# Optimization experiments

Hardware: AMD Instinct MI355X
Metric: run time of the kernel (lower is better)

Reference implementation:

```python
import jax, jax.numpy as jnp
import numpy as np

N = 32767      # 2**15 - 1 nodes: complete binary tree, parent(i) = (i-1)//2
IN = 512       # in_channels
H = 256        # hidden_dim
OUT = 1        # output_dim
DEPTH = 15     # number of topological levels (static)


def setup_inputs() -> dict:
    key = jax.random.key(0)
    ks = jax.random.split(key, 8)
    x = jax.random.normal(ks[0], (N, IN), dtype=jnp.float32)
    # complete binary tree edge list: edge_index[0]=child, edge_index[1]=parent
    src = jnp.arange(1, N, dtype=jnp.int32)
    dst = (src - 1) // 2
    edge_index = jnp.stack([src, dst])  # [2, N-1]
    s = 1.0 / np.sqrt(H)  # torch LSTMCell/Linear default uniform init scale
    W_ih = jax.random.uniform(ks[1], (4 * H, IN), minval=-s, maxval=s, dtype=jnp.float32)
    W_hh = jax.random.uniform(ks[2], (4 * H, H), minval=-s, maxval=s, dtype=jnp.float32)
    b_ih = jax.random.uniform(ks[3], (4 * H,), minval=-s, maxval=s, dtype=jnp.float32)
    b_hh = jax.random.uniform(ks[4], (4 * H,), minval=-s, maxval=s, dtype=jnp.float32)
    W_fc = jax.random.uniform(ks[5], (OUT, H), minval=-s, maxval=s, dtype=jnp.float32)
    b_fc = jax.random.uniform(ks[6], (OUT,), minval=-s, maxval=s, dtype=jnp.float32)
    return {"x": x, "edge_index": edge_index, "W_ih": W_ih, "W_hh": W_hh,
            "b_ih": b_ih, "b_hh": b_hh, "W_fc": W_fc, "b_fc": b_fc}


def reference(x, edge_index, W_ih, W_hh, b_ih, b_hh, W_fc, b_fc):
    src, dst = edge_index[0], edge_index[1]
    # children count per parent (matches torch children_count loop)
    cnt = jax.ops.segment_sum(jnp.ones_like(src, dtype=x.dtype), dst, num_segments=N)
    cnt = jnp.maximum(cnt, 1.0)[:, None]  # [N,1]; leaves get zero child state anyway
    h = jnp.zeros((N, H), dtype=x.dtype)
    c = jnp.zeros((N, H), dtype=x.dtype)
    # topological sweep: deepest level first (children processed before parents)
    for d in range(DEPTH - 1, -1, -1):
        lo = 2 ** d - 1
        hi = min(2 ** (d + 1) - 1, N)  # level d node index range (static)
        # mean of already-computed child h/c states, gathered via edge list
        mean_h = jax.ops.segment_sum(h[src], dst, num_segments=N)[lo:hi] / cnt[lo:hi]
        mean_c = jax.ops.segment_sum(c[src], dst, num_segments=N)[lo:hi] / cnt[lo:hi]
        # torch LSTMCell: gates in (i, f, g, o) order
        gates = x[lo:hi] @ W_ih.T + b_ih + mean_h @ W_hh.T + b_hh  # [n_level, 4H]
        i, f, g, o = jnp.split(gates, 4, axis=-1)
        i, f, o = jax.nn.sigmoid(i), jax.nn.sigmoid(f), jax.nn.sigmoid(o)
        g = jnp.tanh(g)
        c_new = f * mean_c + i * g
        h_new = o * jnp.tanh(c_new)
        h = h.at[lo:hi].set(h_new)
        c = c.at[lo:hi].set(c_new)
    pooled = jnp.mean(h, axis=0, keepdims=True)  # [1, H]
    out = pooled @ W_fc.T + b_fc                 # [1, 1]
    return out.squeeze(-1)                       # [1]
```

## Files before the change

### kernel.cpp

```cpp
#include <hip/hip_runtime.h>
#include <math.h>


#define N_NODES 32767
#define N_LEAF0 16383
#define IN_C    512
#define H_C     256

typedef __bf16 bf16x8 __attribute__((ext_vector_type(8)));
typedef __bf16 bf16x4 __attribute__((ext_vector_type(4)));
typedef float  f32x4  __attribute__((ext_vector_type(4)));

__device__ __forceinline__ void gload_lds16(const void* g, void* l) {
    __builtin_amdgcn_global_load_lds(
        (const __attribute__((address_space(1))) unsigned int*)g,
        (__attribute__((address_space(3))) unsigned int*)l,
        16, 0, 0);
}

__device__ __forceinline__ float fast_rcp(float x) { return __builtin_amdgcn_rcpf(x); }
__device__ __forceinline__ float sigm(float x)     { return fast_rcp(1.f + __expf(-x)); }
__device__ __forceinline__ float tanh_fast(float x){ return 2.f * fast_rcp(1.f + __expf(-2.f * x)) - 1.f; }

__global__ __launch_bounds__(256)
void conv_weights(const float* __restrict__ wih, const float* __restrict__ whh,
                  __bf16* __restrict__ wihb, __bf16* __restrict__ whh2)
{
    const int i = blockIdx.x * 256 + threadIdx.x;
    const float* src; __bf16* dst; float scale; int j;
    if (i < 65536) { src = wih; dst = wihb; scale = 1.0f; j = i; }
    else           { src = whh; dst = whh2; scale = 0.5f; j = i - 65536; }
    const float4* s4 = (const float4*)src;
    const float4 a = s4[2 * j];
    const float4 b = s4[2 * j + 1];
    bf16x8 o;
    o[0] = (__bf16)(scale * a.x); o[1] = (__bf16)(scale * a.y);
    o[2] = (__bf16)(scale * a.z); o[3] = (__bf16)(scale * a.w);
    o[4] = (__bf16)(scale * b.x); o[5] = (__bf16)(scale * b.y);
    o[6] = (__bf16)(scale * b.z); o[7] = (__bf16)(scale * b.w);
    *(bf16x8*)(dst + 8 * j) = o;
}

__global__ __launch_bounds__(256, 2)
void bulk_xw(const float* __restrict__ x,
             const __bf16* __restrict__ wihb,
             const float* __restrict__ b_ih,
             const float* __restrict__ b_hh,
             __bf16* __restrict__ hb,
             __bf16* __restrict__ cb_,
             __bf16* __restrict__ gx)
{
    __shared__ __bf16 As[16 * 64 * 32];

    const int t    = threadIdx.x;
    const int lane = t & 63;
    const int wv   = t >> 6;
    const int quad = lane >> 4;
    const int l15  = lane & 15;
    const int m0   = blockIdx.x * 64;

    {
        const int r  = t >> 2;
        const int ks = (t & 3) * 128;
        const int node = min(m0 + r, N_NODES - 1);
        const float* xr = x + (size_t)node * IN_C + ks;
#pragma unroll
        for (int j = 0; j < 16; ++j) {
            const int k = ks + j * 8;
            const float4 a = *(const float4*)(xr + j * 8);
            const float4 b = *(const float4*)(xr + j * 8 + 4);
            bf16x8 o;
            o[0] = (__bf16)a.x; o[1] = (__bf16)a.y; o[2] = (__bf16)a.z; o[3] = (__bf16)a.w;
            o[4] = (__bf16)b.x; o[5] = (__bf16)b.y; o[6] = (__bf16)b.z; o[7] = (__bf16)b.w;
            *(bf16x8*)(As + (k >> 5) * 2048 + r * 32 + (k & 31)) = o;
        }
    }
    __syncthreads();

    for (int sp = 0; sp < 4; ++sp) {
        const int s  = sp * 4 + wv;
        const int CH = s * 16 + l15;
        float bs[4];
#pragma unroll
        for (int q = 0; q < 4; ++q) bs[q] = b_ih[q * H_C + CH] + b_hh[q * H_C + CH];

        f32x4 acc[4][4];
#pragma unroll
        for (int mi = 0; mi < 4; ++mi)
#pragma unroll
            for (int ni = 0; ni < 4; ++ni) acc[mi][ni] = (f32x4)0.f;

#pragma unroll 4
        for (int kc = 0; kc < 16; ++kc) {
            bf16x8 af[4], bfr[4];
#pragma unroll
            for (int mi = 0; mi < 4; ++mi)
                af[mi] = *(const bf16x8*)(As + kc * 2048 + (mi * 16 + l15) * 32 + quad * 8);
#pragma unroll
            for (int ni = 0; ni < 4; ++ni) {
                const int grow = ni * 256 + s * 16 + l15;
                bfr[ni] = *(const bf16x8*)(wihb + (size_t)grow * IN_C + kc * 32 + quad * 8);
            }
#pragma unroll
            for (int mi = 0; mi < 4; ++mi)
#pragma unroll
                for (int ni = 0; ni < 4; ++ni)
                    acc[mi][ni] = __builtin_amdgcn_mfma_f32_16x16x32_bf16(
                        af[mi], bfr[ni], acc[mi][ni], 0, 0, 0);
        }

#pragma unroll
        for (int mi = 0; mi < 4; ++mi) {
#pragma unroll
            for (int r = 0; r < 4; ++r) {
                const int m = m0 + mi * 16 + quad * 4 + r;
                if (m >= N_NODES) continue;
                if (m >= N_LEAF0) {
                    const float gi = sigm(acc[mi][0][r] + bs[0]);
                    const float gg = tanh_fast(acc[mi][2][r] + bs[2]);
                    const float go = sigm(acc[mi][3][r] + bs[3]);
                    const float cn = gi * gg;
                    const float hn = go * tanh_fast(cn);
                    cb_[(size_t)m * H_C + CH] = (__bf16)cn;
                    hb[(size_t)m * H_C + CH] = (__bf16)hn;
                } else {
                    bf16x4 g4;
#pragma unroll
                    for (int q = 0; q < 4; ++q) g4[q] = (__bf16)acc[mi][q][r];
                    *(bf16x4*)(gx + (size_t)m * 1024 + CH * 4) = g4;
                }
            }
        }
    }
}

__global__ __launch_bounds__(256)
void level_hw(const __bf16* __restrict__ whh2,
              const float* __restrict__ b_ih,
              const float* __restrict__ b_hh,
              const __bf16* __restrict__ gx,
              __bf16* __restrict__ hb,
              __bf16* __restrict__ cb_,
              int lo, int n)
{
    __shared__ __bf16 Bfull[8 * 128 * 32];

    const int t    = threadIdx.x;
    const int lane = t & 63;
    const int wv   = t >> 6;
    const int wm   = wv >> 1;
    const int wn   = wv & 1;
    const int quad = lane >> 4;
    const int l15  = lane & 15;
    const int bx   = blockIdx.x;
    const int cb   = bx & 7;
    const int m0   = (bx >> 3) * 128;

#pragma unroll
    for (int kc = 0; kc < 8; ++kc) {
#pragma unroll
        for (int e = 0; e < 2; ++e) {
            const int chunk = wv * 2 + e;
            const int nl    = chunk * 16 + (lane >> 2);
            const int q     = (nl >> 4) & 3;
            const int cc    = (nl & 15) + ((nl >> 6) << 4);
            const int grow  = q * H_C + cb * 32 + cc;
            const void* g = (const char*)(whh2 + grow * H_C + kc * 32) + (lane & 3) * 16;
            gload_lds16(g, (char*)Bfull + kc * 8192 + chunk * 1024);
        }
    }
    __syncthreads();

    f32x4 acc[4][4];
#pragma unroll
    for (int mi = 0; mi < 4; ++mi)
#pragma unroll
        for (int ni = 0; ni < 4; ++ni) acc[mi][ni] = (f32x4)0.f;

    size_t abase[4];
#pragma unroll
    for (int mi = 0; mi < 4; ++mi) {
        const int node = lo + m0 + wm * 64 + mi * 16 + l15;
        abase[mi] = (size_t)(2 * node + 1) * H_C;
    }

#pragma unroll
    for (int kc = 0; kc < 16; ++kc) {
        bf16x8 af[4], bfr[4];
#pragma unroll
        for (int mi = 0; mi < 4; ++mi)
            af[mi] = *(const bf16x8*)(hb + abase[mi] + kc * 32 + quad * 8);
#pragma unroll
        for (int ni = 0; ni < 4; ++ni)
            bfr[ni] = *(const bf16x8*)(Bfull + (kc & 7) * 4096 +
                                       (wn * 64 + ni * 16 + l15) * 32 + quad * 8);
#pragma unroll
        for (int mi = 0; mi < 4; ++mi)
#pragma unroll
            for (int ni = 0; ni < 4; ++ni)
                acc[mi][ni] = __builtin_amdgcn_mfma_f32_16x16x32_bf16(
                    af[mi], bfr[ni], acc[mi][ni], 0, 0, 0);
    }

    const int CH = cb * 32 + wn * 16 + l15;
    const float bs0 = b_ih[0 * H_C + CH] + b_hh[0 * H_C + CH];
    const float bs1 = b_ih[1 * H_C + CH] + b_hh[1 * H_C + CH];
    const float bs2 = b_ih[2 * H_C + CH] + b_hh[2 * H_C + CH];
    const float bs3 = b_ih[3 * H_C + CH] + b_hh[3 * H_C + CH];

#pragma unroll
    for (int mi = 0; mi < 4; ++mi) {
#pragma unroll
        for (int r = 0; r < 4; ++r) {
            const int m = m0 + wm * 64 + mi * 16 + quad * 4 + r;
            if (m < n) {
                const int node = lo + m;
                const bf16x4 g4 = *(const bf16x4*)(gx + (size_t)node * 1024 + CH * 4);
                const float gi = sigm(acc[mi][0][r] + (float)g4[0] + bs0);
                const float gf = sigm(acc[mi][1][r] + (float)g4[1] + bs1);
                const float gt = tanh_fast(acc[mi][2][r] + (float)g4[2] + bs2);
                const float go = sigm(acc[mi][3][r] + (float)g4[3] + bs3);
                const float mc = 0.5f * ((float)cb_[(size_t)(2 * node + 1) * H_C + CH] +
                                         (float)cb_[(size_t)(2 * node + 2) * H_C + CH]);
                const float cn = gf * mc + gi * gt;
                const float hn = go * tanh_fast(cn);
                cb_[(size_t)node * H_C + CH] = (__bf16)cn;
                hb[(size_t)node * H_C + CH] = (__bf16)hn;
            }
        }
    }
}

__global__ __launch_bounds__(256)
void levels_tail(const __bf16* __restrict__ whh2,
                 const float* __restrict__ b_ih,
                 const float* __restrict__ b_hh,
                 const __bf16* __restrict__ gx,
                 __bf16* __restrict__ hb,
                 __bf16* __restrict__ cb_,
                 int* __restrict__ bar)
{
    const int t    = threadIdx.x;
    const int lane = t & 63;
    const int wv   = t >> 6;
    const int wm   = wv >> 1;
    const int wn   = wv & 1;
    const int quad = lane >> 4;
    const int l15  = lane & 15;
    const int b    = blockIdx.x;
    const int slab = b & 7;
    const int mg   = b >> 3;

    const int CH = slab * 32 + wn * 16 + l15;
    const float bs0 = b_ih[0 * H_C + CH] + b_hh[0 * H_C + CH];
    const float bs1 = b_ih[1 * H_C + CH] + b_hh[1 * H_C + CH];
    const float bs2 = b_ih[2 * H_C + CH] + b_hh[2 * H_C + CH];
    const float bs3 = b_ih[3 * H_C + CH] + b_hh[3 * H_C + CH];

    int target = 0;

    for (int d = 9; d >= 0; --d) {
        const int n  = 1 << d;
        const int lo = n - 1;
        if (mg * 64 < n) {
            const int m0 = mg * 64;

            f32x4 acc[2][4];
#pragma unroll
            for (int mi = 0; mi < 2; ++mi)
#pragma unroll
                for (int ni = 0; ni < 4; ++ni) acc[mi][ni] = (f32x4)0.f;

            size_t abase[2];
#pragma unroll
            for (int mi = 0; mi < 2; ++mi) {
                const int node = lo + m0 + wm * 32 + mi * 16 + l15;
                abase[mi] = (size_t)(2 * node + 1) * H_C;
            }

#pragma unroll 4
            for (int kc = 0; kc < 16; ++kc) {
                bf16x8 af[2], bfr[4];
#pragma unroll
                for (int mi = 0; mi < 2; ++mi)
                    af[mi] = *(const bf16x8*)(hb + abase[mi] + kc * 32 + quad * 8);
#pragma unroll
                for (int ni = 0; ni < 4; ++ni) {
                    const int grow = ni * H_C + CH;
                    bfr[ni] = *(const bf16x8*)(whh2 + (size_t)grow * H_C +
                                               (kc & 7) * 32 + quad * 8);
                }
#pragma unroll
                for (int mi = 0; mi < 2; ++mi)
#pragma unroll
                    for (int ni = 0; ni < 4; ++ni)
                        acc[mi][ni] = __builtin_amdgcn_mfma_f32_16x16x32_bf16(
                            af[mi], bfr[ni], acc[mi][ni], 0, 0, 0);
            }

#pragma unroll
            for (int mi = 0; mi < 2; ++mi) {
#pragma unroll
                for (int r = 0; r < 4; ++r) {
                    const int m = m0 + wm * 32 + mi * 16 + quad * 4 + r;
                    if (m < n) {
                        const int node = lo + m;
                        const bf16x4 g4 = *(const bf16x4*)(gx + (size_t)node * 1024 + CH * 4);
                        const float gi = sigm(acc[mi][0][r] + (float)g4[0] + bs0);
                        const float gf = sigm(acc[mi][1][r] + (float)g4[1] + bs1);
                        const float gt = tanh_fast(acc[mi][2][r] + (float)g4[2] + bs2);
                        const float go = sigm(acc[mi][3][r] + (float)g4[3] + bs3);
                        const float mc = 0.5f * ((float)cb_[(size_t)(2 * node + 1) * H_C + CH] +
                                                 (float)cb_[(size_t)(2 * node + 2) * H_C + CH]);
                        const float cn = gf * mc + gi * gt;
                        const float hn = go * tanh_fast(cn);
                        cb_[(size_t)node * H_C + CH] = (__bf16)cn;
                        hb[(size_t)node * H_C + CH] = (__bf16)hn;
                    }
                }
            }
        }

        if (d > 0) {
            __syncthreads();
            target += 64;
            if (t == 0) {
                __threadfence();
                atomicAdd(bar, 1);
                while (__hip_atomic_load(bar, __ATOMIC_RELAXED,
                                         __HIP_MEMORY_SCOPE_AGENT) < target)
                    __builtin_amdgcn_s_sleep(8);
                __threadfence();
            }
            __syncthreads();
        }
    }
}

__global__ __launch_bounds__(256)
void reduce_rows(const __bf16* __restrict__ hb, float* __restrict__ part)
{
    const int tcol = threadIdx.x;
    const int b = blockIdx.x;
    float s = 0.f;
    for (int r = 0; r < 128; ++r) {
        const int row = b * 128 + r;
        if (row < N_NODES) s += (float)hb[(size_t)row * H_C + tcol];
    }
    part[b * H_C + tcol] = s;
}

__global__ __launch_bounds__(256)
void reduce_final(const float* __restrict__ part,
                  const float* __restrict__ W_fc,
                  const float* __restrict__ b_fc,
                  float* __restrict__ out)
{
    __shared__ float sm[256];
    const int t = threadIdx.x;
    float s = 0.f;
    for (int j = 0; j < 256; ++j) s += part[j * H_C + t];
    s = s * (1.0f / (float)N_NODES) * W_fc[t];
    sm[t] = s;
    __syncthreads();
    for (int st = 128; st > 0; st >>= 1) {
        if (t < st) sm[t] += sm[t + st];
        __syncthreads();
    }
    if (t == 0) out[0] = sm[0] + b_fc[0];
}

extern "C" void kernel_launch(void* const* d_in, const int* in_sizes, int n_in,
                              void* d_out, int out_size, void* d_ws, size_t ws_size,
                              hipStream_t stream)
{
    const float* x    = (const float*)d_in[0];
    const float* W_ih = (const float*)d_in[2];
    const float* W_hh = (const float*)d_in[3];
    const float* b_ih = (const float*)d_in[4];
    const float* b_hh = (const float*)d_in[5];
    const float* W_fc = (const float*)d_in[6];
    const float* b_fc = (const float*)d_in[7];
    float* out = (float*)d_out;

    char* w = (char*)d_ws;
    __bf16* hb   = (__bf16*)w;  w += (size_t)N_NODES * H_C * 2;
    __bf16* cb_  = (__bf16*)w;  w += (size_t)N_NODES * H_C * 2;
    __bf16* gx   = (__bf16*)w;  w += (size_t)N_LEAF0 * 1024 * 2;
    __bf16* wihb = (__bf16*)w;  w += (size_t)4 * H_C * IN_C * 2;
    __bf16* whh2 = (__bf16*)w;  w += (size_t)4 * H_C * H_C * 2;
    float*  part = (float*)w;   w += (size_t)256 * H_C * 4;
    int*    bar  = (int*)w;

    hipMemsetAsync(bar, 0, sizeof(int), stream);

    conv_weights<<<384, 256, 0, stream>>>(W_ih, W_hh, wihb, whh2);

    bulk_xw<<<512, 256, 0, stream>>>(x, wihb, b_ih, b_hh, hb, cb_, gx);

    for (int d = 13; d >= 10; --d) {
        const int n  = 1 << d;
        const int lo = n - 1;
        const int nm = n / 128;
        level_hw<<<8 * nm, 256, 0, stream>>>(whh2, b_ih, b_hh, gx, hb, cb_, lo, n);
    }

    levels_tail<<<64, 256, 0, stream>>>(whh2, b_ih, b_hh, gx, hb, cb_, bar);

    reduce_rows<<<256, 256, 0, stream>>>(hb, part);
    reduce_final<<<1, 256, 0, stream>>>(part, W_fc, b_fc, out);
}
```

Before: 455.8 us.

## Fold level 10 into persistent tail kernel and use relaxed atomics instead of fences

Level 10 now runs inside the persistent levels_tail kernel, which launches 128 blocks instead of 64, so one fewer separate level_hw launch is needed. The grid barrier drops its __threadfence calls and sleeps for a shorter interval. Cross-block visibility of h/c now relies on agent-scope relaxed atomic loads and stores of the bf16 state. This cuts launch and fence overhead, but relaxed atomics without fences give weak ordering guarantees, and the split 8-byte and 2-byte atomic accesses may be less efficient than plain vector loads.

```diff
diff --git a/kernel.cpp b/kernel.cpp
--- a/kernel.cpp
+++ b/kernel.cpp
@@ -10,6 +10,9 @@
 typedef __bf16 bf16x8 __attribute__((ext_vector_type(8)));
 typedef __bf16 bf16x4 __attribute__((ext_vector_type(4)));
 typedef float  f32x4  __attribute__((ext_vector_type(4)));
+
+union U64B { unsigned long long u; bf16x4 v; };
+union U16B { unsigned short u; __bf16 b; };
 
 __device__ __forceinline__ void gload_lds16(const void* g, void* l) {
     __builtin_amdgcn_global_load_lds(
@@ -21,6 +24,28 @@
 __device__ __forceinline__ float fast_rcp(float x) { return __builtin_amdgcn_rcpf(x); }
 __device__ __forceinline__ float sigm(float x)     { return fast_rcp(1.f + __expf(-x)); }
 __device__ __forceinline__ float tanh_fast(float x){ return 2.f * fast_rcp(1.f + __expf(-2.f * x)) - 1.f; }
+
+__device__ __forceinline__ bf16x8 aload16(const __bf16* p) {
+    U64B a, b;
+    a.u = __hip_atomic_load((const unsigned long long*)p,
+                            __ATOMIC_RELAXED, __HIP_MEMORY_SCOPE_AGENT);
+    b.u = __hip_atomic_load((const unsigned long long*)(p + 4),
+                            __ATOMIC_RELAXED, __HIP_MEMORY_SCOPE_AGENT);
+    bf16x8 r;
+    r[0]=a.v[0]; r[1]=a.v[1]; r[2]=a.v[2]; r[3]=a.v[3];
+    r[4]=b.v[0]; r[5]=b.v[1]; r[6]=b.v[2]; r[7]=b.v[3];
+    return r;
+}
+__device__ __forceinline__ float aload_bf16(const __bf16* p) {
+    U16B u; u.u = __hip_atomic_load((const unsigned short*)p,
+                                    __ATOMIC_RELAXED, __HIP_MEMORY_SCOPE_AGENT);
+    return (float)u.b;
+}
+__device__ __forceinline__ void astore_bf16(__bf16* p, float v) {
+    U16B u; u.b = (__bf16)v;
+    __hip_atomic_store((unsigned short*)p, u.u,
+                       __ATOMIC_RELAXED, __HIP_MEMORY_SCOPE_AGENT);
+}
 
 __global__ __launch_bounds__(256)
 void conv_weights(const float* __restrict__ wih, const float* __restrict__ whh,
@@ -259,7 +284,7 @@
 
     int target = 0;
 
-    for (int d = 9; d >= 0; --d) {
+    for (int d = 10; d >= 0; --d) {
         const int n  = 1 << d;
         const int lo = n - 1;
         if (mg * 64 < n) {
@@ -283,7 +308,7 @@
                 bf16x8 af[2], bfr[4];
 #pragma unroll
                 for (int mi = 0; mi < 2; ++mi)
-                    af[mi] = *(const bf16x8*)(hb + abase[mi] + kc * 32 + quad * 8);
+                    af[mi] = aload16(hb + abase[mi] + kc * 32 + quad * 8);
 #pragma unroll
                 for (int ni = 0; ni < 4; ++ni) {
                     const int grow = ni * H_C + CH;
@@ -310,12 +335,13 @@
                         const float gf = sigm(acc[mi][1][r] + (float)g4[1] + bs1);
                         const float gt = tanh_fast(acc[mi][2][r] + (float)g4[2] + bs2);
                         const float go = sigm(acc[mi][3][r] + (float)g4[3] + bs3);
-                        const float mc = 0.5f * ((float)cb_[(size_t)(2 * node + 1) * H_C + CH] +
-                                                 (float)cb_[(size_t)(2 * node + 2) * H_C + CH]);
+                        const float mc = 0.5f *
+                            (aload_bf16(cb_ + (size_t)(2 * node + 1) * H_C + CH) +
+                             aload_bf16(cb_ + (size_t)(2 * node + 2) * H_C + CH));
                         const float cn = gf * mc + gi * gt;
                         const float hn = go * tanh_fast(cn);
-                        cb_[(size_t)node * H_C + CH] = (__bf16)cn;
-                        hb[(size_t)node * H_C + CH] = (__bf16)hn;
+                        astore_bf16(cb_ + (size_t)node * H_C + CH, cn);
+                        astore_bf16(hb + (size_t)node * H_C + CH, hn);
                     }
                 }
             }
@@ -323,14 +349,12 @@
 
         if (d > 0) {
             __syncthreads();
-            target += 64;
+            target += 128;
             if (t == 0) {
-                __threadfence();
                 atomicAdd(bar, 1);
                 while (__hip_atomic_load(bar, __ATOMIC_RELAXED,
                                          __HIP_MEMORY_SCOPE_AGENT) < target)
-                    __builtin_amdgcn_s_sleep(8);
-                __threadfence();
+                    __builtin_amdgcn_s_sleep(2);
             }
             __syncthreads();
         }
@@ -398,14 +422,14 @@
 
     bulk_xw<<<512, 256, 0, stream>>>(x, wihb, b_ih, b_hh, hb, cb_, gx);
 
-    for (int d = 13; d >= 10; --d) {
+    for (int d = 13; d >= 11; --d) {
         const int n  = 1 << d;
         const int lo = n - 1;
         const int nm = n / 128;
         level_hw<<<8 * nm, 256, 0, stream>>>(whh2, b_ih, b_hh, gx, hb, cb_, lo, n);
     }
 
-    levels_tail<<<64, 256, 0, stream>>>(whh2, b_ih, b_hh, gx, hb, cb_, bar);
+    levels_tail<<<128, 256, 0, stream>>>(whh2, b_ih, b_hh, gx, hb, cb_, bar);
 
     reduce_rows<<<256, 256, 0, stream>>>(hb, part);
     reduce_final<<<1, 256, 0, stream>>>(part, W_fc, b_fc, out);
```

Result: slower. 484.3 us (+6.2%).

## Process tree levels as independent subtrees per block instead of per-level launches

Applied to the files above, without the earlier changes.

Replaces the four per-level launches and the grid-barrier tail kernel with a subtree decomposition. Each of 128 blocks handles its own subtree rooted at level 7 through levels 13 to 7, staging child h rows in LDS. A single 1024-thread block then finishes levels 6 to 0. This removes launch overhead and the atomic grid barrier, but the mid kernel now uses only 128 blocks and loops over all 8 column slabs serially, reading W_hh from global memory. That risks underusing the GPU on the wide levels (8192 nodes at level 13) that previously ran with many blocks.

```diff
diff --git a/kernel.cpp b/kernel.cpp
--- a/kernel.cpp
+++ b/kernel.cpp
@@ -6,6 +6,7 @@
 #define N_LEAF0 16383
 #define IN_C    512
 #define H_C     256
+#define AST     520
 
 typedef __bf16 bf16x8 __attribute__((ext_vector_type(8)));
 typedef __bf16 bf16x4 __attribute__((ext_vector_type(4)));
@@ -134,87 +135,56 @@
     }
 }
 
-__global__ __launch_bounds__(256)
-void level_hw(const __bf16* __restrict__ whh2,
-              const float* __restrict__ b_ih,
-              const float* __restrict__ b_hh,
-              const __bf16* __restrict__ gx,
-              __bf16* __restrict__ hb,
-              __bf16* __restrict__ cb_,
-              int lo, int n)
-{
-    __shared__ __bf16 Bfull[8 * 128 * 32];
-
-    const int t    = threadIdx.x;
-    const int lane = t & 63;
-    const int wv   = t >> 6;
-    const int wm   = wv >> 1;
-    const int wn   = wv & 1;
-    const int quad = lane >> 4;
-    const int l15  = lane & 15;
-    const int bx   = blockIdx.x;
-    const int cb   = bx & 7;
-    const int m0   = (bx >> 3) * 128;
-
-#pragma unroll
-    for (int kc = 0; kc < 8; ++kc) {
-#pragma unroll
-        for (int e = 0; e < 2; ++e) {
-            const int chunk = wv * 2 + e;
-            const int nl    = chunk * 16 + (lane >> 2);
-            const int q     = (nl >> 4) & 3;
-            const int cc    = (nl & 15) + ((nl >> 6) << 4);
-            const int grow  = q * H_C + cb * 32 + cc;
-            const void* g = (const char*)(whh2 + grow * H_C + kc * 32) + (lane & 3) * 16;
-            gload_lds16(g, (char*)Bfull + kc * 8192 + chunk * 1024);
-        }
-    }
-    __syncthreads();
-
-    f32x4 acc[4][4];
-#pragma unroll
-    for (int mi = 0; mi < 4; ++mi)
+__device__ __forceinline__ void level_unit(
+    const __bf16* __restrict__ As,
+    const __bf16* __restrict__ whh2,
+    const float* __restrict__ b_ih, const float* __restrict__ b_hh,
+    const __bf16* __restrict__ gx,
+    __bf16* __restrict__ hb, __bf16* __restrict__ cb_,
+    int slab, int first, int rows,
+    int wm, int wn, int quad, int l15)
+{
+    const int CH = slab * 32 + wn * 16 + l15;
+
+    f32x4 acc[2][4];
+#pragma unroll
+    for (int mi = 0; mi < 2; ++mi)
 #pragma unroll
         for (int ni = 0; ni < 4; ++ni) acc[mi][ni] = (f32x4)0.f;
 
-    size_t abase[4];
-#pragma unroll
-    for (int mi = 0; mi < 4; ++mi) {
-        const int node = lo + m0 + wm * 64 + mi * 16 + l15;
-        abase[mi] = (size_t)(2 * node + 1) * H_C;
-    }
-
-#pragma unroll
+#pragma unroll 4
     for (int kc = 0; kc < 16; ++kc) {
-        bf16x8 af[4], bfr[4];
-#pragma unroll
-        for (int mi = 0; mi < 4; ++mi)
-            af[mi] = *(const bf16x8*)(hb + abase[mi] + kc * 32 + quad * 8);
-#pragma unroll
-        for (int ni = 0; ni < 4; ++ni)
-            bfr[ni] = *(const bf16x8*)(Bfull + (kc & 7) * 4096 +
-                                       (wn * 64 + ni * 16 + l15) * 32 + quad * 8);
-#pragma unroll
-        for (int mi = 0; mi < 4; ++mi)
+        bf16x8 af[2], bfr[4];
+#pragma unroll
+        for (int mi = 0; mi < 2; ++mi)
+            af[mi] = *(const bf16x8*)(As + (wm * 32 + mi * 16 + l15) * AST +
+                                      kc * 32 + quad * 8);
+#pragma unroll
+        for (int ni = 0; ni < 4; ++ni) {
+            const int grow = ni * H_C + CH;
+            bfr[ni] = *(const bf16x8*)(whh2 + (size_t)grow * H_C +
+                                       (kc & 7) * 32 + quad * 8);
+        }
+#pragma unroll
+        for (int mi = 0; mi < 2; ++mi)
 #pragma unroll
             for (int ni = 0; ni < 4; ++ni)
                 acc[mi][ni] = __builtin_amdgcn_mfma_f32_16x16x32_bf16(
                     af[mi], bfr[ni], acc[mi][ni], 0, 0, 0);
     }
 
-    const int CH = cb * 32 + wn * 16 + l15;
     const float bs0 = b_ih[0 * H_C + CH] + b_hh[0 * H_C + CH];
     const float bs1 = b_ih[1 * H_C + CH] + b_hh[1 * H_C + CH];
     const float bs2 = b_ih[2 * H_C + CH] + b_hh[2 * H_C + CH];
     const float bs3 = b_ih[3 * H_C + CH] + b_hh[3 * H_C + CH];
 
 #pragma unroll
-    for (int mi = 0; mi < 4; ++mi) {
+    for (int mi = 0; mi < 2; ++mi) {
 #pragma unroll
         for (int r = 0; r < 4; ++r) {
-            const int m = m0 + wm * 64 + mi * 16 + quad * 4 + r;
-            if (m < n) {
-                const int node = lo + m;
+            const int m = wm * 32 + mi * 16 + quad * 4 + r;
+            if (m < rows) {
+                const int node = first + m;
                 const bf16x4 g4 = *(const bf16x4*)(gx + (size_t)node * 1024 + CH * 4);
                 const float gi = sigm(acc[mi][0][r] + (float)g4[0] + bs0);
                 const float gf = sigm(acc[mi][1][r] + (float)g4[1] + bs1);
@@ -232,14 +202,15 @@
 }
 
 __global__ __launch_bounds__(256)
-void levels_tail(const __bf16* __restrict__ whh2,
+void subtree_mid(const __bf16* __restrict__ whh2,
                  const float* __restrict__ b_ih,
                  const float* __restrict__ b_hh,
                  const __bf16* __restrict__ gx,
                  __bf16* __restrict__ hb,
-                 __bf16* __restrict__ cb_,
-                 int* __restrict__ bar)
-{
+                 __bf16* __restrict__ cb_)
+{
+    __shared__ __bf16 As[64 * AST];
+
     const int t    = threadIdx.x;
     const int lane = t & 63;
     const int wv   = t >> 6;
@@ -247,93 +218,73 @@
     const int wn   = wv & 1;
     const int quad = lane >> 4;
     const int l15  = lane & 15;
-    const int b    = blockIdx.x;
-    const int slab = b & 7;
-    const int mg   = b >> 3;
-
-    const int CH = slab * 32 + wn * 16 + l15;
-    const float bs0 = b_ih[0 * H_C + CH] + b_hh[0 * H_C + CH];
-    const float bs1 = b_ih[1 * H_C + CH] + b_hh[1 * H_C + CH];
-    const float bs2 = b_ih[2 * H_C + CH] + b_hh[2 * H_C + CH];
-    const float bs3 = b_ih[3 * H_C + CH] + b_hh[3 * H_C + CH];
-
-    int target = 0;
-
-    for (int d = 9; d >= 0; --d) {
-        const int n  = 1 << d;
-        const int lo = n - 1;
-        if (mg * 64 < n) {
-            const int m0 = mg * 64;
-
-            f32x4 acc[2][4];
-#pragma unroll
-            for (int mi = 0; mi < 2; ++mi)
-#pragma unroll
-                for (int ni = 0; ni < 4; ++ni) acc[mi][ni] = (f32x4)0.f;
-
-            size_t abase[2];
-#pragma unroll
-            for (int mi = 0; mi < 2; ++mi) {
-                const int node = lo + m0 + wm * 32 + mi * 16 + l15;
-                abase[mi] = (size_t)(2 * node + 1) * H_C;
-            }
-
-#pragma unroll 4
-            for (int kc = 0; kc < 16; ++kc) {
-                bf16x8 af[2], bfr[4];
-#pragma unroll
-                for (int mi = 0; mi < 2; ++mi)
-                    af[mi] = *(const bf16x8*)(hb + abase[mi] + kc * 32 + quad * 8);
-#pragma unroll
-                for (int ni = 0; ni < 4; ++ni) {
-                    const int grow = ni * H_C + CH;
-                    bfr[ni] = *(const bf16x8*)(whh2 + (size_t)grow * H_C +
-                                               (kc & 7) * 32 + quad * 8);
-                }
-#pragma unroll
-                for (int mi = 0; mi < 2; ++mi)
-#pragma unroll
-                    for (int ni = 0; ni < 4; ++ni)
-                        acc[mi][ni] = __builtin_amdgcn_mfma_f32_16x16x32_bf16(
-                            af[mi], bfr[ni], acc[mi][ni], 0, 0, 0);
-            }
-
-#pragma unroll
-            for (int mi = 0; mi < 2; ++mi) {
-#pragma unroll
-                for (int r = 0; r < 4; ++r) {
-                    const int m = m0 + wm * 32 + mi * 16 + quad * 4 + r;
-                    if (m < n) {
-                        const int node = lo + m;
-                        const bf16x4 g4 = *(const bf16x4*)(gx + (size_t)node * 1024 + CH * 4);
-                        const float gi = sigm(acc[mi][0][r] + (float)g4[0] + bs0);
-                        const float gf = sigm(acc[mi][1][r] + (float)g4[1] + bs1);
-                        const float gt = tanh_fast(acc[mi][2][r] + (float)g4[2] + bs2);
-                        const float go = sigm(acc[mi][3][r] + (float)g4[3] + bs3);
-                        const float mc = 0.5f * ((float)cb_[(size_t)(2 * node + 1) * H_C + CH] +
-                                                 (float)cb_[(size_t)(2 * node + 2) * H_C + CH]);
-                        const float cn = gf * mc + gi * gt;
-                        const float hn = go * tanh_fast(cn);
-                        cb_[(size_t)node * H_C + CH] = (__bf16)cn;
-                        hb[(size_t)node * H_C + CH] = (__bf16)hn;
-                    }
-                }
-            }
-        }
-
-        if (d > 0) {
-            __syncthreads();
-            target += 64;
-            if (t == 0) {
-                __threadfence();
-                atomicAdd(bar, 1);
-                while (__hip_atomic_load(bar, __ATOMIC_RELAXED,
-                                         __HIP_MEMORY_SCOPE_AGENT) < target)
-                    __builtin_amdgcn_s_sleep(8);
-                __threadfence();
-            }
-            __syncthreads();
-        }
+    const int root = 127 + blockIdx.x;
+
+    for (int ld = 13; ld >= 7; --ld) {
+        const int sh    = ld - 7;
+        const int rows  = 1 << sh;
+        const int first = ((root + 1) << sh) - 1;
+
+        {
+            const int row = t >> 2;
+            const int qtr = t & 3;
+            const __bf16* src = hb + (size_t)(2 * (first + row) + 1) * H_C + qtr * 128;
+            __bf16* dst = As + row * AST + qtr * 128;
+#pragma unroll
+            for (int j = 0; j < 16; ++j)
+                *(bf16x8*)(dst + j * 8) = *(const bf16x8*)(src + j * 8);
+        }
+        __syncthreads();
+
+        for (int slab = 0; slab < 8; ++slab)
+            level_unit(As, whh2, b_ih, b_hh, gx, hb, cb_,
+                       slab, first, rows, wm, wn, quad, l15);
+
+        __syncthreads();
+    }
+}
+
+__global__ __launch_bounds__(1024)
+void subtree_top(const __bf16* __restrict__ whh2,
+                 const float* __restrict__ b_ih,
+                 const float* __restrict__ b_hh,
+                 const __bf16* __restrict__ gx,
+                 __bf16* __restrict__ hb,
+                 __bf16* __restrict__ cb_)
+{
+    __shared__ __bf16 As[64 * AST];
+
+    const int t    = threadIdx.x;
+    const int lane = t & 63;
+    const int wv   = t >> 6;
+    const int grp  = wv >> 2;
+    const int wq   = wv & 3;
+    const int wm   = wq >> 1;
+    const int wn   = wq & 1;
+    const int quad = lane >> 4;
+    const int l15  = lane & 15;
+
+    for (int ld = 6; ld >= 0; --ld) {
+        const int rows  = 1 << ld;
+        const int first = rows - 1;
+
+        {
+            const int row = t >> 4;
+            const int cb0 = (t & 15) * 32;
+            const __bf16* src = hb + (size_t)(2 * (first + row) + 1) * H_C + cb0;
+            __bf16* dst = As + row * AST + cb0;
+#pragma unroll
+            for (int j = 0; j < 4; ++j)
+                *(bf16x8*)(dst + j * 8) = *(const bf16x8*)(src + j * 8);
+        }
+        __syncthreads();
+
+#pragma unroll
+        for (int sp = 0; sp < 2; ++sp)
+            level_unit(As, whh2, b_ih, b_hh, gx, hb, cb_,
+                       grp + sp * 4, first, rows, wm, wn, quad, l15);
+
+        __syncthreads();
     }
 }
 
@@ -389,23 +340,15 @@
     __bf16* gx   = (__bf16*)w;  w += (size_t)N_LEAF0 * 1024 * 2;
     __bf16* wihb = (__bf16*)w;  w += (size_t)4 * H_C * IN_C * 2;
     __bf16* whh2 = (__bf16*)w;  w += (size_t)4 * H_C * H_C * 2;
-    float*  part = (float*)w;   w += (size_t)256 * H_C * 4;
-    int*    bar  = (int*)w;
-
-    hipMemsetAsync(bar, 0, sizeof(int), stream);
+    float*  part = (float*)w;
 
     conv_weights<<<384, 256, 0, stream>>>(W_ih, W_hh, wihb, whh2);
 
     bulk_xw<<<512, 256, 0, stream>>>(x, wihb, b_ih, b_hh, hb, cb_, gx);
 
-    for (int d = 13; d >= 10; --d) {
-        const int n  = 1 << d;
-        const int lo = n - 1;
-        const int nm = n / 128;
-        level_hw<<<8 * nm, 256, 0, stream>>>(whh2, b_ih, b_hh, gx, hb, cb_, lo, n);
-    }
-
-    levels_tail<<<64, 256, 0, stream>>>(whh2, b_ih, b_hh, gx, hb, cb_, bar);
+    subtree_mid<<<128, 256, 0, stream>>>(whh2, b_ih, b_hh, gx, hb, cb_);
+
+    subtree_top<<<1, 1024, 0, stream>>>(whh2, b_ih, b_hh, gx, hb, cb_);
 
     reduce_rows<<<256, 256, 0, stream>>>(hb, part);
     reduce_final<<<1, 256, 0, stream>>>(part, W_fc, b_fc, out);
```

Result: slower. 1.170 ms (+156.8%).
